# Optimization experiments

Measured on AMD Instinct MI355X. Metric: run time of the kernel, lower is better.

The kernel has to match this reference:

```python
import jax, jax.numpy as jnp
import numpy as np

C = 512
CQK = C // 8  # 64


def setup_inputs() -> dict:
    key = jax.random.key(0)
    ks = jax.random.split(key, 7)
    s = 0.02
    x = jax.random.normal(ks[0], (4, C, 64, 64), dtype=jnp.float32)
    Wq = jax.random.normal(ks[1], (CQK, C), dtype=jnp.float32) * s
    bq = jnp.zeros((CQK,), dtype=jnp.float32)
    Wk = jax.random.normal(ks[2], (CQK, C), dtype=jnp.float32) * s
    bk = jnp.zeros((CQK,), dtype=jnp.float32)
    Wv = jax.random.normal(ks[3], (C, C), dtype=jnp.float32) * s
    bv = jnp.zeros((C,), dtype=jnp.float32)
    return {"x": x, "Wq": Wq, "bq": bq, "Wk": Wk, "bk": bk, "Wv": Wv, "bv": bv}


def reference(x, Wq, bq, Wk, bk, Wv, bv):
    B, Cc, W, H = x.shape
    N = W * H
    xf = x.reshape(B, Cc, N)  # [B, C, N]
    # 1x1 convs are channel-wise matmuls
    q = jnp.einsum('oc,bcn->bon', Wq, xf) + bq[None, :, None]  # [B, CQK, N]
    k = jnp.einsum('oc,bcn->bon', Wk, xf) + bk[None, :, None]  # [B, CQK, N]
    v = jnp.einsum('oc,bcn->bon', Wv, xf) + bv[None, :, None]  # [B, C, N]
    # attention[b, i, j] = softmax_j(q_i . k_j)
    scores = jnp.einsum('bqi,bqj->bij', q, k)  # [B, N, N]
    attn = jax.nn.softmax(scores, axis=-1)
    # out[b, c, i] = sum_j v[b, c, j] * attn[b, i, j]
    out = jnp.einsum('bcj,bij->bci', v, attn)
    return out.reshape(B, Cc, W, H) + x
```

## Files before the change

### kernel.cpp

```cpp
#include <hip/hip_runtime.h>


typedef __attribute__((ext_vector_type(8))) short bf16x8;
typedef __attribute__((ext_vector_type(4))) float f32x4;

#define MFMA16(A, B, C) __builtin_amdgcn_mfma_f32_16x16x32_bf16((A), (B), (C), 0, 0, 0)
#define MFMA8(A, B, C) __builtin_amdgcn_mfma_f32_16x16x32_fp8_fp8((long)(A), (long)(B), (C), 0, 0, 0)

__device__ __forceinline__ ushort f2bf(float f) {
  uint u = __builtin_bit_cast(uint, f);
  u = (u + 0x7FFFu + ((u >> 16) & 1u)) >> 16;
  return (ushort)u;
}

__device__ __forceinline__ void gload_lds16(const void* g, void* l) {
  __builtin_amdgcn_global_load_lds(
      (const __attribute__((address_space(1))) void*)g,
      (__attribute__((address_space(3))) void*)l, 16, 0, 0);
}

__device__ __forceinline__ void lds_barrier() {
  __builtin_amdgcn_sched_barrier(0);
  asm volatile("s_waitcnt lgkmcnt(0)" ::: "memory");
  __builtin_amdgcn_s_barrier();
  __builtin_amdgcn_sched_barrier(0);
}

__global__ void wconv(const float* __restrict__ Wq, const float* __restrict__ Wk,
                      const float* __restrict__ Wv, ushort* __restrict__ Wb) {
  const int row = blockIdx.x;
  const int t = threadIdx.x;
  const float* src = row < 64 ? Wq + (size_t)row * 512
                   : row < 128 ? Wk + (size_t)(row - 64) * 512
                               : Wv + (size_t)(row - 128) * 512;
  const float4 f = *reinterpret_cast<const float4*>(src + t * 4);
  ushort4 u;
  u.x = f2bf(f.x); u.y = f2bf(f.y); u.z = f2bf(f.z); u.w = f2bf(f.w);
  *reinterpret_cast<ushort4*>(Wb + (size_t)row * 512 + t * 4) = u;
}

__global__ __launch_bounds__(512, 1) void qkv_fused(
    const float* __restrict__ x, const ushort* __restrict__ Wb,
    const float* __restrict__ bq, const float* __restrict__ bk,
    const float* __restrict__ bv,
    ushort* __restrict__ q, ushort* __restrict__ k, uchar* __restrict__ v) {
  __shared__ ushort xT[64][72];

  const int bid = blockIdx.x;
  const int xcd = bid & 7;
  const int b = xcd >> 1;
  const int n0 = ((bid >> 3) + ((xcd & 1) << 5)) * 64;
  const int tid = threadIdx.x;
  const int w = tid >> 6, l = tid & 63;
  const int l15 = l & 15, l16 = l >> 4;

  const float* xb = x + (size_t)b * 512 * 4096 + n0;

  float xr[8];
#define LOADX(CH0)                                              \
  _Pragma("unroll") for (int p = 0; p < 8; ++p)                 \
      xr[p] = xb[((size_t)((CH0) + w * 8 + p)) * 4096 + l];

  LOADX(0);

  const f32x4 fz = {0.f, 0.f, 0.f, 0.f};
  f32x4 acc[4][5];
#pragma unroll
  for (int a = 0; a < 4; ++a)
#pragma unroll
    for (int o = 0; o < 5; ++o) acc[a][o] = fz;

  for (int ck = 0; ck < 8; ++ck) {
    bf16x8 xw;
#pragma unroll
    for (int p = 0; p < 8; ++p) xw[p] = (short)f2bf(xr[p]);
    *reinterpret_cast<bf16x8*>(&xT[l][w * 8]) = xw;
    lds_barrier();
    if (ck < 7) {
      const int c1 = (ck + 1) * 64;
      LOADX(c1);
    }
#pragma unroll
    for (int kk = 0; kk < 2; ++kk) {
      bf16x8 a[4];
#pragma unroll
      for (int nf = 0; nf < 4; ++nf)
        a[nf] = *reinterpret_cast<const bf16x8*>(&xT[nf * 16 + l15][kk * 32 + l16 * 8]);
#pragma unroll
      for (int oi = 0; oi < 5; ++oi) {
        const bf16x8 bw = *reinterpret_cast<const bf16x8*>(
            &Wb[(size_t)(w * 80 + oi * 16 + l15) * 512 + ck * 64 + kk * 32 + l16 * 8]);
#pragma unroll
        for (int nf = 0; nf < 4; ++nf) acc[nf][oi] = MFMA16(a[nf], bw, acc[nf][oi]);
      }
    }
    lds_barrier();
  }

#pragma unroll
  for (int oi = 0; oi < 5; ++oi) {
    const int obase = w * 80 + oi * 16;
    const int orow = obase + l15;
    if (obase < 64) {
      const float bias = bq[orow];
      ushort* dq = q + ((size_t)b * 4096 + n0) * 64;
#pragma unroll
      for (int nf = 0; nf < 4; ++nf)
#pragma unroll
        for (int r = 0; r < 4; ++r)
          dq[(size_t)(nf * 16 + l16 * 4 + r) * 64 + orow] = f2bf(acc[nf][oi][r] + bias);
    } else if (obase < 128) {
      const float bias = bk[orow - 64];
      ushort* dk = k + ((size_t)b * 4096 + n0) * 64;
#pragma unroll
      for (int nf = 0; nf < 4; ++nf)
#pragma unroll
        for (int r = 0; r < 4; ++r)
          dk[(size_t)(nf * 16 + l16 * 4 + r) * 64 + (orow - 64)] = f2bf(acc[nf][oi][r] + bias);
    } else {
      const int c = orow - 128;
      const float bias = bv[c];
#pragma unroll
      for (int nf = 0; nf < 4; ++nf) {
        uint u = 0;
        u = __builtin_amdgcn_cvt_pk_fp8_f32(acc[nf][oi][0] + bias, acc[nf][oi][1] + bias, u, false);
        u = __builtin_amdgcn_cvt_pk_fp8_f32(acc[nf][oi][2] + bias, acc[nf][oi][3] + bias, u, true);
        *reinterpret_cast<uint*>(&v[((size_t)b * 512 + c) * 4096 + n0 + nf * 16 + l16 * 4]) = u;
      }
    }
  }
}

__global__ __launch_bounds__(128, 1) void attn_kernel(
    const float* __restrict__ x, const ushort* __restrict__ q,
    const ushort* __restrict__ k, const uchar* __restrict__ v,
    float* __restrict__ out) {
  __shared__ uchar vbuf[2][32768];
  __shared__ uchar Pb[2][16 * 72];
  __shared__ float l_buf[2][16];

  const int bid = blockIdx.x;
  const int xcd = bid & 7;
  const int b = xcd >> 1;
  const int i0 = ((bid >> 3) + ((xcd & 1) << 6)) * 32;
  const int tid = threadIdx.x;
  const int w = tid >> 6, l = tid & 63;
  const int l15 = l & 15, l16 = l >> 4;

  const int i0w = i0 + w * 16;
  const ushort* kb = k + (size_t)b * 4096 * 64;
  const uchar* vg = v + (size_t)b * 512 * 4096;
  uchar* Pw = &Pb[w][0];

  bf16x8 qf0, qf1;
  {
    const ushort* qp = q + ((size_t)b * 4096 + i0w + l15) * 64 + l16 * 8;
    qf0 = *reinterpret_cast<const bf16x8*>(qp);
    qf1 = *reinterpret_cast<const bf16x8*>(qp + 32);
  }

  const int sc_off = w * 16 + (l >> 2);
  const int sswz = (2 * (l & 3)) ^ (sc_off & 6);
  const uchar* vstage = vg + (size_t)sc_off * 4096 + sswz * 8;

  const int voff0 = l15 * 64 + ((l16 ^ (l15 & 6)) * 8);
  const int voff1 = l15 * 64 + (((4 + l16) ^ (l15 & 6)) * 8);

  const f32x4 fz = {0.f, 0.f, 0.f, 0.f};
  f32x4 acc[32];
#pragma unroll
  for (int ct = 0; ct < 32; ++ct) acc[ct] = fz;
  float l_acc = 0.f;

  bf16x8 kc[4][2], kn[4][2];

#define STAGE(J0, NB)                                                         \
  {                                                                           \
    const uchar* _s = vstage + (J0);                                          \
    _Pragma("unroll") for (int rho = 0; rho < 16; ++rho)                      \
        gload_lds16(_s + (size_t)rho * 32 * 4096,                             \
                    &vbuf[NB][rho * 2048 + w * 1024]);                        \
  }

#define KLOAD(J0, DST)                                                        \
  {                                                                           \
    _Pragma("unroll") for (int tt = 0; tt < 4; ++tt) {                        \
      const ushort* kp = kb + (size_t)((J0) + tt * 16 + l15) * 64 + l16 * 8;  \
      DST[tt][0] = *reinterpret_cast<const bf16x8*>(kp);                      \
      DST[tt][1] = *reinterpret_cast<const bf16x8*>(kp + 32);                 \
    }                                                                         \
  }

#define ITER(T, KC, KN)                                                       \
  {                                                                           \
                \
    __builtin_amdgcn_sched_barrier(0);                                        \
    __builtin_amdgcn_s_barrier();                                             \
    __builtin_amdgcn_sched_barrier(0);                                        \
    const int _jn = (((T) + 1) & 63) * 64;                                    \
    STAGE(_jn, ((T) + 1) & 1);                                                \
    KLOAD(_jn, KN);                                                           \
    __builtin_amdgcn_sched_barrier(0);                                        \
    asm volatile("s_waitcnt vmcnt(24)" ::: "memory");                         \
    __builtin_amdgcn_s_barrier();      \
    __builtin_amdgcn_sched_barrier(0);                                        \
                                              \
    _Pragma("unroll") for (int tt = 0; tt < 4; ++tt) {                        \
      f32x4 s = fz;                                                           \
      s = MFMA16(KC[tt][0], qf0, s);                                          \
      s = MFMA16(KC[tt][1], qf1, s);                                          \
      const float p0 = __expf(s[0] - 5.f);                                    \
      const float p1 = __expf(s[1] - 5.f);                                    \
      const float p2 = __expf(s[2] - 5.f);                                    \
      const float p3 = __expf(s[3] - 5.f);                                    \
      l_acc += (p0 + p1) + (p2 + p3);                                         \
      uint pu = 0;                                                            \
      pu = __builtin_amdgcn_cvt_pk_fp8_f32(p0, p1, pu, false);                \
      pu = __builtin_amdgcn_cvt_pk_fp8_f32(p2, p3, pu, true);                 \
      *reinterpret_cast<uint*>(&Pw[l15 * 72 + tt * 16 + l16 * 4]) = pu;       \
    }                                                                         \
          \
    asm volatile("s_waitcnt lgkmcnt(0)" ::: "memory");                        \
    __builtin_amdgcn_sched_barrier(0);                                        \
            \
    const ulong pa0 = *reinterpret_cast<const ulong*>(&Pw[l15 * 72 + l16 * 8]);      \
    const ulong pa1 = *reinterpret_cast<const ulong*>(&Pw[l15 * 72 + 32 + l16 * 8]); \
    const uchar* vB = vbuf[(T) & 1];                                          \
    __builtin_amdgcn_s_setprio(1);                                            \
    _Pragma("unroll") for (int ct = 0; ct < 32; ++ct) {                       \
      const ulong v0 = *reinterpret_cast<const ulong*>(vB + ct * 1024 + voff0); \
      const ulong v1 = *reinterpret_cast<const ulong*>(vB + ct * 1024 + voff1); \
      acc[ct] = MFMA8(pa0, v0, acc[ct]);                                      \
      acc[ct] = MFMA8(pa1, v1, acc[ct]);                                      \
    }                                                                         \
    __builtin_amdgcn_s_setprio(0);                                            \
  }

  STAGE(0, 0);
  KLOAD(0, kc);
  for (int t = 0; t < 64; t += 2) {
    ITER(t, kc, kn);
    ITER(t + 1, kn, kc);
  }
  asm volatile("s_waitcnt vmcnt(0)" ::: "memory");

  l_acc += __shfl_xor(l_acc, 16);
  l_acc += __shfl_xor(l_acc, 32);
  if (l < 16) l_buf[w][l] = l_acc;
  __builtin_amdgcn_sched_barrier(0);
  asm volatile("s_waitcnt lgkmcnt(0)" ::: "memory");
  __builtin_amdgcn_sched_barrier(0);

  float linv[4];
#pragma unroll
  for (int r = 0; r < 4; ++r) linv[r] = 1.f / l_buf[w][l16 * 4 + r];

#pragma unroll
  for (int ct = 0; ct < 32; ++ct) {
    const int c = ct * 16 + l15;
    const size_t idx = ((size_t)b * 512 + c) * 4096 + i0w + l16 * 4;
    const float4 xr = *reinterpret_cast<const float4*>(&x[idx]);
    float4 o;
    o.x = acc[ct][0] * linv[0] + xr.x;
    o.y = acc[ct][1] * linv[1] + xr.y;
    o.z = acc[ct][2] * linv[2] + xr.z;
    o.w = acc[ct][3] * linv[3] + xr.w;
    *reinterpret_cast<float4*>(&out[idx]) = o;
  }
}

extern "C" void kernel_launch(void* const* d_in, const int* in_sizes, int n_in,
                              void* d_out, int out_size, void* d_ws, size_t ws_size,
                              hipStream_t stream) {
  const float* x  = (const float*)d_in[0];
  const float* Wq = (const float*)d_in[1];
  const float* bq = (const float*)d_in[2];
  const float* Wk = (const float*)d_in[3];
  const float* bk = (const float*)d_in[4];
  const float* Wv = (const float*)d_in[5];
  const float* bv = (const float*)d_in[6];
  float* out = (float*)d_out;

  ushort* qws = (ushort*)d_ws;
  ushort* kws = qws + (size_t)4 * 4096 * 64;
  uchar*  vws = (uchar*)(kws + (size_t)4 * 4096 * 64);
  ushort* wb  = (ushort*)(vws + (size_t)4 * 512 * 4096);

  wconv<<<dim3(640), 128, 0, stream>>>(Wq, Wk, Wv, wb);
  qkv_fused<<<dim3(256), 512, 0, stream>>>(x, wb, bq, bk, bv, qws, kws, vws);
  attn_kernel<<<dim3(512), 128, 0, stream>>>(x, qws, kws, vws, out);
}
```

Baseline: 177.3 us.

## Split attention block across four waves with channel halves and alternating softmax duty

```diff
diff --git a/kernel.cpp b/kernel.cpp
--- a/kernel.cpp
+++ b/kernel.cpp
@@ -131,13 +131,13 @@
   }
 }
 
-__global__ __launch_bounds__(128, 1) void attn_kernel(
+__global__ __launch_bounds__(256, 2) void attn_kernel(
     const float* __restrict__ x, const ushort* __restrict__ q,
     const ushort* __restrict__ k, const uchar* __restrict__ v,
     float* __restrict__ out) {
   __shared__ uchar vbuf[2][32768];
-  __shared__ uchar Pb[2][16 * 72];
-  __shared__ float l_buf[2][16];
+  __shared__ uchar Pp[2][2][16 * 72];
+  __shared__ float l_part[2][2][16];
 
   const int bid = blockIdx.x;
   const int xcd = bid & 7;
@@ -146,11 +146,11 @@
   const int tid = threadIdx.x;
   const int w = tid >> 6, l = tid & 63;
   const int l15 = l & 15, l16 = l >> 4;
-
-  const int i0w = i0 + w * 16;
+  const int rg = w & 1, ch = w >> 1;
+  const int i0w = i0 + rg * 16;
+
   const ushort* kb = k + (size_t)b * 4096 * 64;
   const uchar* vg = v + (size_t)b * 512 * 4096;
-  uchar* Pw = &Pb[w][0];
 
   bf16x8 qf0, qf1;
   {
@@ -159,75 +159,86 @@
     qf1 = *reinterpret_cast<const bf16x8*>(qp + 32);
   }
 
-  const int sc_off = w * 16 + (l >> 2);
-  const int sswz = (2 * (l & 3)) ^ (sc_off & 6);
-  const uchar* vstage = vg + (size_t)sc_off * 4096 + sswz * 8;
+  const int cbase = tid >> 2;
+  const int slot = tid & 3;
+  const uchar* vstage = vg + (size_t)cbase * 4096 + (size_t)(((2 * slot) ^ (cbase & 6)) * 8);
+  uchar* ldst = &vbuf[0][0] + cbase * 64 + slot * 16;
 
   const int voff0 = l15 * 64 + ((l16 ^ (l15 & 6)) * 8);
   const int voff1 = l15 * 64 + (((4 + l16) ^ (l15 & 6)) * 8);
+  const int choff = ch * 16384;
 
   const f32x4 fz = {0.f, 0.f, 0.f, 0.f};
-  f32x4 acc[32];
-#pragma unroll
-  for (int ct = 0; ct < 32; ++ct) acc[ct] = fz;
+  f32x4 acc[16];
+#pragma unroll
+  for (int ct = 0; ct < 16; ++ct) acc[ct] = fz;
   float l_acc = 0.f;
 
-  bf16x8 kc[4][2], kn[4][2];
+  bf16x8 kc[4][2];
 
 #define STAGE(J0, NB)                                                         \
   {                                                                           \
     const uchar* _s = vstage + (J0);                                          \
-    _Pragma("unroll") for (int rho = 0; rho < 16; ++rho)                      \
-        gload_lds16(_s + (size_t)rho * 32 * 4096,                             \
-                    &vbuf[NB][rho * 2048 + w * 1024]);                        \
-  }
-
-#define KLOAD(J0, DST)                                                        \
+    uchar* _d = ldst + (NB) * 32768;                                          \
+    _Pragma("unroll") for (int r = 0; r < 8; ++r)                             \
+        gload_lds16(_s + (size_t)r * 64 * 4096, _d + r * 4096);               \
+  }
+
+#define KLOAD(J0)                                                             \
   {                                                                           \
     _Pragma("unroll") for (int tt = 0; tt < 4; ++tt) {                        \
       const ushort* kp = kb + (size_t)((J0) + tt * 16 + l15) * 64 + l16 * 8;  \
-      DST[tt][0] = *reinterpret_cast<const bf16x8*>(kp);                      \
-      DST[tt][1] = *reinterpret_cast<const bf16x8*>(kp + 32);                 \
+      kc[tt][0] = *reinterpret_cast<const bf16x8*>(kp);                       \
+      kc[tt][1] = *reinterpret_cast<const bf16x8*>(kp + 32);                  \
     }                                                                         \
   }
 
-#define ITER(T, KC, KN)                                                       \
+#define ITER(T, PAR)                                                          \
   {                                                                           \
-                \
-    __builtin_amdgcn_sched_barrier(0);                                        \
-    __builtin_amdgcn_s_barrier();                                             \
+       \
+    __builtin_amdgcn_sched_barrier(0);                                        \
+    asm volatile("s_barrier" ::: "memory");                                   \
     __builtin_amdgcn_sched_barrier(0);                                        \
     const int _jn = (((T) + 1) & 63) * 64;                                    \
+    if (ch != (PAR)) KLOAD(_jn);             \
     STAGE(_jn, ((T) + 1) & 1);                                                \
-    KLOAD(_jn, KN);                                                           \
-    __builtin_amdgcn_sched_barrier(0);                                        \
-    asm volatile("s_waitcnt vmcnt(24)" ::: "memory");                         \
-    __builtin_amdgcn_s_barrier();      \
-    __builtin_amdgcn_sched_barrier(0);                                        \
-                                              \
-    _Pragma("unroll") for (int tt = 0; tt < 4; ++tt) {                        \
-      f32x4 s = fz;                                                           \
-      s = MFMA16(KC[tt][0], qf0, s);                                          \
-      s = MFMA16(KC[tt][1], qf1, s);                                          \
-      const float p0 = __expf(s[0] - 5.f);                                    \
-      const float p1 = __expf(s[1] - 5.f);                                    \
-      const float p2 = __expf(s[2] - 5.f);                                    \
-      const float p3 = __expf(s[3] - 5.f);                                    \
-      l_acc += (p0 + p1) + (p2 + p3);                                         \
-      uint pu = 0;                                                            \
-      pu = __builtin_amdgcn_cvt_pk_fp8_f32(p0, p1, pu, false);                \
-      pu = __builtin_amdgcn_cvt_pk_fp8_f32(p2, p3, pu, true);                 \
-      *reinterpret_cast<uint*>(&Pw[l15 * 72 + tt * 16 + l16 * 4]) = pu;       \
+    __builtin_amdgcn_sched_barrier(0);                                        \
+    if (ch == (PAR)) {                                                        \
+      asm volatile("s_waitcnt vmcnt(8)" ::: "memory");                        \
+    } else {                                                                  \
+      asm volatile("s_waitcnt vmcnt(16)" ::: "memory");                       \
     }                                                                         \
-          \
-    asm volatile("s_waitcnt lgkmcnt(0)" ::: "memory");                        \
-    __builtin_amdgcn_sched_barrier(0);                                        \
-            \
-    const ulong pa0 = *reinterpret_cast<const ulong*>(&Pw[l15 * 72 + l16 * 8]);      \
-    const ulong pa1 = *reinterpret_cast<const ulong*>(&Pw[l15 * 72 + 32 + l16 * 8]); \
-    const uchar* vB = vbuf[(T) & 1];                                          \
+    __builtin_amdgcn_sched_barrier(0);                                        \
+    if (ch == (PAR)) {            \
+      uchar* Pw = &Pp[(T) & 1][rg][0];                                        \
+      _Pragma("unroll") for (int tt = 0; tt < 4; ++tt) {                      \
+        f32x4 s = fz;                                                         \
+        s = MFMA16(kc[tt][0], qf0, s);                                        \
+        s = MFMA16(kc[tt][1], qf1, s);                                        \
+        const float p0 = __expf(s[0] - 5.f);                                  \
+        const float p1 = __expf(s[1] - 5.f);                                  \
+        const float p2 = __expf(s[2] - 5.f);                                  \
+        const float p3 = __expf(s[3] - 5.f);                                  \
+        l_acc += (p0 + p1) + (p2 + p3);                                       \
+        uint pu = 0;                                                          \
+        pu = __builtin_amdgcn_cvt_pk_fp8_f32(p0, p1, pu, false);              \
+        pu = __builtin_amdgcn_cvt_pk_fp8_f32(p2, p3, pu, true);               \
+        *reinterpret_cast<uint*>(&Pw[l15 * 72 + tt * 16 + l16 * 4]) = pu;     \
+      }                                                                       \
+                       \
+      asm volatile("s_waitcnt lgkmcnt(0)" ::: "memory");                      \
+      __builtin_amdgcn_sched_barrier(0);                                      \
+    }                                                                         \
+                   \
+    asm volatile("s_barrier" ::: "memory");                                   \
+    __builtin_amdgcn_sched_barrier(0);                                        \
+              \
+    const uchar* Pr = &Pp[(T) & 1][rg][0];                                    \
+    const ulong pa0 = *reinterpret_cast<const ulong*>(&Pr[l15 * 72 + l16 * 8]);      \
+    const ulong pa1 = *reinterpret_cast<const ulong*>(&Pr[l15 * 72 + 32 + l16 * 8]); \
+    const uchar* vB = vbuf[(T) & 1] + choff;                                  \
     __builtin_amdgcn_s_setprio(1);                                            \
-    _Pragma("unroll") for (int ct = 0; ct < 32; ++ct) {                       \
+    _Pragma("unroll") for (int ct = 0; ct < 16; ++ct) {                       \
       const ulong v0 = *reinterpret_cast<const ulong*>(vB + ct * 1024 + voff0); \
       const ulong v1 = *reinterpret_cast<const ulong*>(vB + ct * 1024 + voff1); \
       acc[ct] = MFMA8(pa0, v0, acc[ct]);                                      \
@@ -236,28 +247,27 @@
     __builtin_amdgcn_s_setprio(0);                                            \
   }
 
+  if (ch == 0) KLOAD(0);
   STAGE(0, 0);
-  KLOAD(0, kc);
   for (int t = 0; t < 64; t += 2) {
-    ITER(t, kc, kn);
-    ITER(t + 1, kn, kc);
+    ITER(t, 0);
+    ITER(t + 1, 1);
   }
   asm volatile("s_waitcnt vmcnt(0)" ::: "memory");
 
   l_acc += __shfl_xor(l_acc, 16);
   l_acc += __shfl_xor(l_acc, 32);
-  if (l < 16) l_buf[w][l] = l_acc;
-  __builtin_amdgcn_sched_barrier(0);
-  asm volatile("s_waitcnt lgkmcnt(0)" ::: "memory");
-  __builtin_amdgcn_sched_barrier(0);
+  if (l < 16) l_part[rg][ch][l] = l_acc;
+  lds_barrier();
 
   float linv[4];
 #pragma unroll
-  for (int r = 0; r < 4; ++r) linv[r] = 1.f / l_buf[w][l16 * 4 + r];
-
-#pragma unroll
-  for (int ct = 0; ct < 32; ++ct) {
-    const int c = ct * 16 + l15;
+  for (int r = 0; r < 4; ++r)
+    linv[r] = 1.f / (l_part[rg][0][l16 * 4 + r] + l_part[rg][1][l16 * 4 + r]);
+
+#pragma unroll
+  for (int ct = 0; ct < 16; ++ct) {
+    const int c = ch * 256 + ct * 16 + l15;
     const size_t idx = ((size_t)b * 512 + c) * 4096 + i0w + l16 * 4;
     const float4 xr = *reinterpret_cast<const float4*>(&x[idx]);
     float4 o;
@@ -288,5 +298,5 @@
 
   wconv<<<dim3(640), 128, 0, stream>>>(Wq, Wk, Wv, wb);
   qkv_fused<<<dim3(256), 512, 0, stream>>>(x, wb, bq, bk, bv, qws, kws, vws);
-  attn_kernel<<<dim3(512), 128, 0, stream>>>(x, qws, kws, vws, out);
-}
+  attn_kernel<<<dim3(512), 256, 0, stream>>>(x, qws, kws, vws, out);
+}
```

After: 168.5 us. -5.0%, faster.

## Split attention block into four waves across channel halves, exchange P via shuffles

Applied to the files above, without the earlier changes.

```diff
diff --git a/kernel.cpp b/kernel.cpp
--- a/kernel.cpp
+++ b/kernel.cpp
@@ -131,13 +131,12 @@
   }
 }
 
-__global__ __launch_bounds__(128, 1) void attn_kernel(
+__global__ __launch_bounds__(256, 2) void attn_kernel(
     const float* __restrict__ x, const ushort* __restrict__ q,
     const ushort* __restrict__ k, const uchar* __restrict__ v,
     float* __restrict__ out) {
   __shared__ uchar vbuf[2][32768];
-  __shared__ uchar Pb[2][16 * 72];
-  __shared__ float l_buf[2][16];
+  __shared__ float l_sm[4][16];
 
   const int bid = blockIdx.x;
   const int xcd = bid & 7;
@@ -146,11 +145,13 @@
   const int tid = threadIdx.x;
   const int w = tid >> 6, l = tid & 63;
   const int l15 = l & 15, l16 = l >> 4;
-
-  const int i0w = i0 + w * 16;
+  const int hi = l >> 5;
+  const int rg = w & 1, ch = w >> 1;
+  const int i0w = i0 + rg * 16;
+  const int c0 = ch * 256;
+
   const ushort* kb = k + (size_t)b * 4096 * 64;
   const uchar* vg = v + (size_t)b * 512 * 4096;
-  uchar* Pw = &Pb[w][0];
 
   bf16x8 qf0, qf1;
   {
@@ -159,17 +160,24 @@
     qf1 = *reinterpret_cast<const bf16x8*>(qp + 32);
   }
 
-  const int sc_off = w * 16 + (l >> 2);
-  const int sswz = (2 * (l & 3)) ^ (sc_off & 6);
-  const uchar* vstage = vg + (size_t)sc_off * 4096 + sswz * 8;
+  const int vrow = tid >> 2;
+  const int vslot = tid & 3;
+  const uchar* vstage = vg + (size_t)vrow * 4096 + (size_t)(((2 * vslot) ^ (vrow & 6)) * 8);
+  uchar* vdst = &vbuf[0][0] + vrow * 64 + vslot * 16;
 
   const int voff0 = l15 * 64 + ((l16 ^ (l15 & 6)) * 8);
-  const int voff1 = l15 * 64 + (((4 + l16) ^ (l15 & 6)) * 8);
+  const int voff1 = l15 * 64 + (((4 ^ l16) ^ (l15 & 6)) * 8);
+  const int choff = ch * 16384;
+
+  const int src0 = l15 + ((l16 & 1) << 5);
+  const int src1 = src0 + 16;
+
+  const ushort* kl = kb + (size_t)l15 * 64 + l16 * 8;
 
   const f32x4 fz = {0.f, 0.f, 0.f, 0.f};
-  f32x4 acc[32];
-#pragma unroll
-  for (int ct = 0; ct < 32; ++ct) acc[ct] = fz;
+  f32x4 acc[16];
+#pragma unroll
+  for (int ct = 0; ct < 16; ++ct) acc[ct] = fz;
   float l_acc = 0.f;
 
   bf16x8 kc[4][2], kn[4][2];
@@ -177,15 +185,15 @@
 #define STAGE(J0, NB)                                                         \
   {                                                                           \
     const uchar* _s = vstage + (J0);                                          \
-    _Pragma("unroll") for (int rho = 0; rho < 16; ++rho)                      \
-        gload_lds16(_s + (size_t)rho * 32 * 4096,                             \
-                    &vbuf[NB][rho * 2048 + w * 1024]);                        \
+    uchar* _d = vdst + (NB) * 32768;                                          \
+    _Pragma("unroll") for (int r = 0; r < 8; ++r)                             \
+        gload_lds16(_s + (size_t)r * 64 * 4096, _d + r * 4096);               \
   }
 
 #define KLOAD(J0, DST)                                                        \
   {                                                                           \
     _Pragma("unroll") for (int tt = 0; tt < 4; ++tt) {                        \
-      const ushort* kp = kb + (size_t)((J0) + tt * 16 + l15) * 64 + l16 * 8;  \
+      const ushort* kp = kl + (size_t)((J0) + tt * 16) * 64;                  \
       DST[tt][0] = *reinterpret_cast<const bf16x8*>(kp);                      \
       DST[tt][1] = *reinterpret_cast<const bf16x8*>(kp + 32);                 \
     }                                                                         \
@@ -193,18 +201,22 @@
 
 #define ITER(T, KC, KN)                                                       \
   {                                                                           \
-                \
-    __builtin_amdgcn_sched_barrier(0);                                        \
-    __builtin_amdgcn_s_barrier();                                             \
-    __builtin_amdgcn_sched_barrier(0);                                        \
-    const int _jn = (((T) + 1) & 63) * 64;                                    \
-    STAGE(_jn, ((T) + 1) & 1);                                                \
-    KLOAD(_jn, KN);                                                           \
-    __builtin_amdgcn_sched_barrier(0);                                        \
-    asm volatile("s_waitcnt vmcnt(24)" ::: "memory");                         \
-    __builtin_amdgcn_s_barrier();      \
-    __builtin_amdgcn_sched_barrier(0);                                        \
-                                              \
+    const int cur = (T) & 1;                                                  \
+    const int jn = (((T) + 1) & 63) * 64;                                     \
+              \
+    __builtin_amdgcn_sched_barrier(0);                                        \
+    asm volatile("s_barrier" ::: "memory");                                   \
+    __builtin_amdgcn_sched_barrier(0);                                        \
+    STAGE(jn, cur ^ 1);                                                       \
+    KLOAD(jn, KN);                                                            \
+         \
+    __builtin_amdgcn_sched_barrier(0);                                        \
+    asm volatile("s_waitcnt vmcnt(16)" ::: "memory");                         \
+    __builtin_amdgcn_sched_barrier(0);                                        \
+    asm volatile("s_barrier" ::: "memory");           \
+    __builtin_amdgcn_sched_barrier(0);                                        \
+                       \
+    uint u[4];                                                                \
     _Pragma("unroll") for (int tt = 0; tt < 4; ++tt) {                        \
       f32x4 s = fz;                                                           \
       s = MFMA16(KC[tt][0], qf0, s);                                          \
@@ -217,17 +229,19 @@
       uint pu = 0;                                                            \
       pu = __builtin_amdgcn_cvt_pk_fp8_f32(p0, p1, pu, false);                \
       pu = __builtin_amdgcn_cvt_pk_fp8_f32(p2, p3, pu, true);                 \
-      *reinterpret_cast<uint*>(&Pw[l15 * 72 + tt * 16 + l16 * 4]) = pu;       \
+      u[tt] = pu;                                                             \
     }                                                                         \
-          \
-    asm volatile("s_waitcnt lgkmcnt(0)" ::: "memory");                        \
-    __builtin_amdgcn_sched_barrier(0);                                        \
-            \
-    const ulong pa0 = *reinterpret_cast<const ulong*>(&Pw[l15 * 72 + l16 * 8]);      \
-    const ulong pa1 = *reinterpret_cast<const ulong*>(&Pw[l15 * 72 + 32 + l16 * 8]); \
-    const uchar* vB = vbuf[(T) & 1];                                          \
+                       \
+    const uint a0 = __shfl(u[0], src0), b0 = __shfl(u[1], src0);              \
+    const uint a1 = __shfl(u[0], src1), b1 = __shfl(u[1], src1);              \
+    const uint e0 = __shfl(u[2], src0), f0 = __shfl(u[3], src0);              \
+    const uint e1 = __shfl(u[2], src1), f1 = __shfl(u[3], src1);              \
+    const ulong pa0 = (ulong)(hi ? b0 : a0) | ((ulong)(hi ? b1 : a1) << 32);  \
+    const ulong pa1 = (ulong)(hi ? f0 : e0) | ((ulong)(hi ? f1 : e1) << 32);  \
+                               \
+    const uchar* vB = &vbuf[cur][0] + choff;                                  \
     __builtin_amdgcn_s_setprio(1);                                            \
-    _Pragma("unroll") for (int ct = 0; ct < 32; ++ct) {                       \
+    _Pragma("unroll") for (int ct = 0; ct < 16; ++ct) {                       \
       const ulong v0 = *reinterpret_cast<const ulong*>(vB + ct * 1024 + voff0); \
       const ulong v1 = *reinterpret_cast<const ulong*>(vB + ct * 1024 + voff1); \
       acc[ct] = MFMA8(pa0, v0, acc[ct]);                                      \
@@ -246,18 +260,18 @@
 
   l_acc += __shfl_xor(l_acc, 16);
   l_acc += __shfl_xor(l_acc, 32);
-  if (l < 16) l_buf[w][l] = l_acc;
+  if (l < 16) l_sm[w][l] = l_acc;
   __builtin_amdgcn_sched_barrier(0);
   asm volatile("s_waitcnt lgkmcnt(0)" ::: "memory");
   __builtin_amdgcn_sched_barrier(0);
 
   float linv[4];
 #pragma unroll
-  for (int r = 0; r < 4; ++r) linv[r] = 1.f / l_buf[w][l16 * 4 + r];
-
-#pragma unroll
-  for (int ct = 0; ct < 32; ++ct) {
-    const int c = ct * 16 + l15;
+  for (int r = 0; r < 4; ++r) linv[r] = 1.f / l_sm[w][l16 * 4 + r];
+
+#pragma unroll
+  for (int ct = 0; ct < 16; ++ct) {
+    const int c = c0 + ct * 16 + l15;
     const size_t idx = ((size_t)b * 512 + c) * 4096 + i0w + l16 * 4;
     const float4 xr = *reinterpret_cast<const float4*>(&x[idx]);
     float4 o;
@@ -288,5 +302,5 @@
 
   wconv<<<dim3(640), 128, 0, stream>>>(Wq, Wk, Wv, wb);
   qkv_fused<<<dim3(256), 512, 0, stream>>>(x, wb, bq, bk, bv, qws, kws, vws);
-  attn_kernel<<<dim3(512), 128, 0, stream>>>(x, qws, kws, vws, out);
-}
+  attn_kernel<<<dim3(512), 256, 0, stream>>>(x, qws, kws, vws, out);
+}
```

Measured after the change: 221.2 us. +24.8%, slower.
